# Kernel tuning notes

Measured on AMD Instinct MI355X. Metric: run time of the kernel, lower is better.

Reference implementation:

```python
import jax, jax.numpy as jnp
import numpy as np

B, T, D = 2, 2048, 2048
H, HKV, DH = 16, 4, 128  # n_heads, n_kv_heads, d_head
EPS = 1e-6


def _rms_norm(t):
    # normalize over last dim, no learned weight (matches F.rms_norm default)
    return t * jax.lax.rsqrt(jnp.mean(t * t, axis=-1, keepdims=True) + EPS)


def _ortho_rope(t, cos, sin):
    # t: (b, h, t, d); unfold(-1,2,2) -> even/odd pairs
    x0 = t[..., 0::2]  # (b,h,t,d/2)
    x1 = t[..., 1::2]
    y0 = x0 * cos - x1 * sin
    y1 = x1 * cos + x0 * sin
    # NOTE: concatenated halves (NOT re-interleaved), faithful to source
    return jnp.concatenate((y0, y1), axis=-1)


def setup_inputs() -> dict:
    key = jax.random.key(0)
    ks = jax.random.split(key, 10)
    return {
        "x": jax.random.normal(ks[0], (B, T, D), jnp.float32),
        "pos_ids": jnp.broadcast_to(jnp.arange(T, dtype=jnp.int64), (B, T)),
        "cos": jax.random.normal(ks[1], (T, DH // 2), jnp.float32),
        "sin": jax.random.normal(ks[2], (T, DH // 2), jnp.float32),
        "v1": jax.random.normal(ks[3], (B, HKV, T, DH), jnp.float32),
        "Wq": jax.random.normal(ks[4], (H * DH, D), jnp.float32) * (D ** -0.5),
        "Wk": jax.random.normal(ks[5], (HKV * DH, D), jnp.float32) * (D ** -0.5),
        "Wv": jax.random.normal(ks[6], (HKV * DH, D), jnp.float32) * (D ** -0.5),
        "Wo": jax.random.normal(ks[7], (D, D), jnp.float32) * (D ** -0.5),
        "gate_w": jax.random.normal(ks[8], (H, H), jnp.float32) * 0.1,
        "v_lamb": jnp.float32(0.5),
    }


def reference(x, pos_ids, cos, sin, v1, Wq, Wk, Wv, Wo, gate_w, v_lamb):
    b, t, _ = x.shape
    # fused QKV projections (Linear, no bias: x @ W.T), split to heads
    q = (x @ Wq.T).reshape(b, t, H, DH).transpose(0, 2, 1, 3)    # (b,H,t,d)
    k = (x @ Wk.T).reshape(b, t, HKV, DH).transpose(0, 2, 1, 3)  # (b,Hkv,t,d)
    v = (x @ Wv.T).reshape(b, t, HKV, DH).transpose(0, 2, 1, 3)
    # value residual: lerp(v, v1, lamb) = v + lamb*(v1 - v)
    v = v + v_lamb * (v1 - v)
    # QK RMSNorm then ortho RoPE
    q = _ortho_rope(_rms_norm(q), cos, sin)
    k = _ortho_rope(_rms_norm(k), cos, sin)
    # kv_cache.upsert modeled as prefill: k,v unchanged, causal block mask
    g = H // HKV  # GQA group size
    k = jnp.repeat(k, g, axis=1)  # (b,H,t,d)
    vfull = jnp.repeat(v, g, axis=1)
    scale = DH ** -0.5
    scores = jnp.einsum('bhqd,bhkd->bhqk', q, k) * scale
    causal = jnp.tril(jnp.ones((t, t), dtype=bool))
    scores = jnp.where(causal, scores, jnp.finfo(scores.dtype).min)
    attn = jax.nn.softmax(scores, axis=-1)
    y = jnp.einsum('bhqk,bhkd->bhqd', attn, vfull)  # (b,H,t,d)
    # per-head sigmoid gate from first n_heads channels of x
    gates = jax.nn.sigmoid(x[..., :H] @ gate_w.T)   # (b,t,H)
    y = y * gates.transpose(0, 2, 1)[..., None]     # (b,H,t,1)
    y = y.transpose(0, 2, 1, 3).reshape(b, t, H * DH)
    out = y @ Wo.T
    return (out, v1)
```

## Files before the change

### kernel.cpp

```cpp
#include <hip/hip_runtime.h>

typedef __bf16 bf16;
typedef __attribute__((ext_vector_type(8))) __bf16 bf16x8;
typedef __attribute__((ext_vector_type(4))) __bf16 bf16x4;
typedef __attribute__((ext_vector_type(4))) float f32x4;
typedef __attribute__((ext_vector_type(4))) short short4v;

#define BB 2
#define TT 2048
#define DD 2048
#define HH 16
#define HKV 4
#define DHD 128
#define NQKV 3072

__device__ __forceinline__ void gl_lds16(const bf16* g, bf16* l) {
    __builtin_amdgcn_global_load_lds(
        (const __attribute__((address_space(1))) void*)g,
        (__attribute__((address_space(3))) void*)l, 16, 0, 0);
}

__global__ void cvt_bf16(const float* __restrict__ src, bf16* __restrict__ dst, int n8) {
    int i = blockIdx.x * 256 + threadIdx.x;
    if (i >= n8) return;
    float4 a = ((const float4*)src)[i * 2];
    float4 b = ((const float4*)src)[i * 2 + 1];
    bf16x8 v;
    v[0] = (bf16)a.x; v[1] = (bf16)a.y; v[2] = (bf16)a.z; v[3] = (bf16)a.w;
    v[4] = (bf16)b.x; v[5] = (bf16)b.y; v[6] = (bf16)b.z; v[7] = (bf16)b.w;
    *(bf16x8*)(dst + (size_t)i * 8) = v;
}

template <int MODE>
__global__ void gemm_bt(const bf16* __restrict__ A, const bf16* __restrict__ Bw,
                        int M, int N, int K,
                        float* __restrict__ Cout,
                        bf16* __restrict__ qb, bf16* __restrict__ kb,
                        bf16* __restrict__ vtb,
                        const float* __restrict__ v1,
                        const float* __restrict__ cosb,
                        const float* __restrict__ sinb,
                        const float* __restrict__ lamp) {
    constexpr int SMEM_ELE = (MODE == 1) ? 17920 : 16384;
    __shared__ bf16 smem[SMEM_ELE];
    bf16* As = smem;
    bf16* Bs = smem + 8192;
    const int tid = threadIdx.x;
    const int w = tid >> 6, lane = tid & 63;
    const int l15 = lane & 15, quad = lane >> 4;

    const int nwg = gridDim.x * gridDim.y;
    int wg = blockIdx.y * gridDim.x + blockIdx.x;
    int swz = (wg & 7) * (nwg >> 3) + (wg >> 3);
    const int bx = swz % gridDim.x, by = swz / gridDim.x;
    const int m0 = by * 128, n0 = bx * 128;
    const int wm = (w & 1) * 64, wn = (w >> 1) * 64;

    f32x4 acc[4][4] = {};
    const int lrow = lane >> 2;
    const int scol = ((lane & 3) ^ ((lane >> 3) & 3)) * 8;
    const int xs = (quad ^ ((l15 >> 1) & 3)) * 8;

    for (int k0 = 0; k0 < K; k0 += 64) {
#pragma unroll
        for (int i = 0; i < 4; i++) {
            int c = w * 4 + i;
            int kc2 = c >> 3, rc = c & 7;
            int row = rc * 16 + lrow;
            int kk = k0 + kc2 * 32 + scol;
            gl_lds16(A + (size_t)(m0 + row) * K + kk, As + c * 512);
            gl_lds16(Bw + (size_t)(n0 + row) * K + kk, Bs + c * 512);
        }
        __syncthreads();
#pragma unroll
        for (int kc2 = 0; kc2 < 2; kc2++) {
            bf16x8 af[4], bfr[4];
#pragma unroll
            for (int mi = 0; mi < 4; mi++)
                af[mi] = *(const bf16x8*)(As + kc2 * 4096 + ((wm >> 4) + mi) * 512 + l15 * 32 + xs);
#pragma unroll
            for (int ni = 0; ni < 4; ni++)
                bfr[ni] = *(const bf16x8*)(Bs + kc2 * 4096 + ((wn >> 4) + ni) * 512 + l15 * 32 + xs);
#pragma unroll
            for (int mi = 0; mi < 4; mi++)
#pragma unroll
                for (int ni = 0; ni < 4; ni++)
                    acc[mi][ni] = __builtin_amdgcn_mfma_f32_16x16x32_bf16(af[mi], bfr[ni], acc[mi][ni], 0, 0, 0);
        }
        __syncthreads();
    }

    if constexpr (MODE == 0) {
#pragma unroll
        for (int mi = 0; mi < 4; mi++)
#pragma unroll
            for (int ni = 0; ni < 4; ni++)
#pragma unroll
                for (int r = 0; r < 4; r++) {
                    int m = m0 + wm + mi * 16 + quad * 4 + r;
                    int n = n0 + wn + ni * 16 + l15;
                    Cout[(size_t)m * N + n] = acc[mi][ni][r];
                }
    } else {
        const int hid = n0 >> 7;
        const int b = m0 >> 11;
        const int t0 = m0 & (TT - 1);
        bf16* ep = smem;

        if (hid < 20) {
            float* ssum = (float*)(smem + 17408);
            float ssq[4][4];
#pragma unroll
            for (int mi = 0; mi < 4; mi++)
#pragma unroll
                for (int r = 0; r < 4; r++) {
                    float s = 0.f;
#pragma unroll
                    for (int ni = 0; ni < 4; ni++) {
                        float v = acc[mi][ni][r];
                        s += v * v;
                    }
                    s += __shfl_xor(s, 1);
                    s += __shfl_xor(s, 2);
                    s += __shfl_xor(s, 4);
                    s += __shfl_xor(s, 8);
                    ssq[mi][r] = s;
                }
            if (l15 == 0) {
#pragma unroll
                for (int mi = 0; mi < 4; mi++)
#pragma unroll
                    for (int r = 0; r < 4; r++)
                        ssum[(wn >> 6) * 128 + wm + mi * 16 + quad * 4 + r] = ssq[mi][r];
            }
            __syncthreads();
            const float QSCALE = 0.08838834764831845f * 1.4426950408889634f;
            float rn[4][4];
#pragma unroll
            for (int mi = 0; mi < 4; mi++)
#pragma unroll
                for (int r = 0; r < 4; r++) {
                    int row = wm + mi * 16 + quad * 4 + r;
                    float ss = ssum[row] + ssum[128 + row];
                    float rv = rsqrtf(ss * (1.f / 128.f) + 1e-6f);
                    if (hid < HH) rv *= QSCALE;
                    rn[mi][r] = rv;
                }
#pragma unroll
            for (int mi = 0; mi < 4; mi++)
#pragma unroll
                for (int ni = 0; ni < 4; ni++)
#pragma unroll
                    for (int r = 0; r < 4; r++) {
                        float sv = acc[mi][ni][r] * rn[mi][r];
                        float pv = __shfl_xor(sv, 1);
                        int nl = wn + ni * 16 + l15;
                        int j = nl >> 1;
                        int tl = wm + mi * 16 + quad * 4 + r;
                        float c = cosb[(size_t)(t0 + tl) * 64 + j];
                        float s = sinb[(size_t)(t0 + tl) * 64 + j];
                        float o = (nl & 1) ? (sv * c + pv * s) : (sv * c - pv * s);
                        int oc = (nl & 1) ? (64 + j) : j;
                        ep[tl * 136 + oc] = (bf16)o;
                    }
            __syncthreads();
            bf16* dst = (hid < HH)
                ? (qb + ((size_t)(b * HH + hid) * TT + t0) * DHD)
                : (kb + ((size_t)(b * HKV + (hid - HH)) * TT + t0) * DHD);
            int tl = tid >> 1, half = tid & 1;
#pragma unroll
            for (int c8 = 0; c8 < 8; c8++)
                *(bf16x8*)(dst + (size_t)tl * DHD + half * 64 + c8 * 8) =
                    *(const bf16x8*)(ep + tl * 136 + half * 64 + c8 * 8);
        } else {
            float lam = lamp[0];
            int vh = hid - 20;
            const float* v1b = v1 + ((size_t)(b * HKV + vh) * TT) * DHD;
#pragma unroll
            for (int mi = 0; mi < 4; mi++)
#pragma unroll
                for (int ni = 0; ni < 4; ni++)
#pragma unroll
                    for (int r = 0; r < 4; r++) {
                        int d = wn + ni * 16 + l15;
                        int tl = wm + mi * 16 + quad * 4 + r;
                        float val = acc[mi][ni][r];
                        float vm = val + lam * (v1b[(size_t)(t0 + tl) * DHD + d] - val);
                        ep[d * 136 + tl] = (bf16)vm;
                    }
            __syncthreads();
            bf16* dstv = vtb + ((size_t)(b * HKV + vh) * DHD) * TT + t0;
            int dd = tid >> 1, half = tid & 1;
#pragma unroll
            for (int c8 = 0; c8 < 8; c8++)
                *(bf16x8*)(dstv + (size_t)dd * TT + half * 64 + c8 * 8) =
                    *(const bf16x8*)(ep + dd * 136 + half * 64 + c8 * 8);
        }
    }
}

__global__ void gatesk(const float* __restrict__ x, const float* __restrict__ gw,
                       float* __restrict__ gates) {
    __shared__ float gws[256];
    gws[threadIdx.x] = gw[threadIdx.x];
    __syncthreads();
    int idx = blockIdx.x * 256 + threadIdx.x;
    int h = idx & 15, token = idx >> 4;
    const float* xr = x + (size_t)token * DD;
    float z = 0.f;
#pragma unroll
    for (int j = 0; j < 16; j++) z += xr[j] * gws[h * 16 + j];
    gates[idx] = 1.f / (1.f + __expf(-z));
}

__global__ __launch_bounds__(512, 2) void fattn(const bf16* __restrict__ qbuf,
                                                const bf16* __restrict__ kbuf,
                                                const bf16* __restrict__ vt,
                                                const float* __restrict__ gates,
                                                bf16* __restrict__ yb) {
    __shared__ bf16 Ks[2][4 * 2048];
    __shared__ bf16 VTs[2][8192];

    const int bid = blockIdx.x;
    const int bh = bid & 31;
    const int g = bid >> 5;
    const int h = bh & 15, b = bh >> 4;
    const int hk = h >> 2;
    const int tid = threadIdx.x, w = tid >> 6, lane = tid & 63;
    const int wq = w & 3, grp = w >> 2;
    const int l15 = lane & 15, quad = lane >> 4;

    const bf16* qbase = qbuf + ((size_t)(b * HH + h) * TT) * DHD;
    const bf16* kbase = kbuf + ((size_t)(b * HKV + hk) * TT) * DHD;
    const bf16* vtbase = vt + ((size_t)(b * HKV + hk) * DHD) * TT;

    const int Tq0 = grp ? (15 - g) : g;
    const int Tq1 = grp ? (16 + g) : (31 - g);
    const int ktmax_blk = 31 - g;

    bf16x8 qf0[4], qf1[4];
#pragma unroll
    for (int kc = 0; kc < 4; kc++) {
        qf0[kc] = *(const bf16x8*)(qbase + (size_t)(Tq0 * 64 + wq * 16 + l15) * DHD + kc * 32 + quad * 8);
        qf1[kc] = *(const bf16x8*)(qbase + (size_t)(Tq1 * 64 + wq * 16 + l15) * DHD + kc * 32 + quad * 8);
    }

    bool dm[4][4];
#pragma unroll
    for (int ni = 0; ni < 4; ni++)
#pragma unroll
        for (int r = 0; r < 4; r++)
            dm[ni][r] = ((ni >> 1) * 32 + quad * 8 + (ni & 1) * 4 + r) > (wq * 16 + l15);

    const int srow = lane >> 2;
    const int gst = (((lane >> 5) & 1) << 1) | ((lane >> 3) & 1);
    const int scg = ((lane & 3) ^ gst) * 8;
    const int vrow = lane >> 3;
    const int vcg = ((lane & 7) ^ ((lane >> 3) & 7)) * 8;

    auto stage = [&](int kt, int buf) {
        if (grp == 0) {
#pragma unroll
            for (int i = 0; i < 4; i++)
                gl_lds16(kbase + (size_t)(kt * 64 + wq * 16 + srow) * DHD + i * 32 + scg,
                         &Ks[buf][i * 2048 + wq * 512]);
        } else {
#pragma unroll
            for (int i = 0; i < 4; i++)
                gl_lds16(vtbase + (size_t)(wq * 32 + i * 8 + vrow) * TT + kt * 64 + vcg,
                         &VTs[buf][wq * 2048 + i * 512]);
        }
    };

    stage(0, 0);

    const int gk = (((l15 >> 2) & 1) << 1) | ((l15 >> 1) & 1);

    f32x4 O0[8] = {}, O1[8] = {};
    float m0 = -INFINITY, l0 = 0.f, m1 = -INFINITY, l1 = 0.f;

    union PW { bf16x4 h[2]; bf16x8 v; };

    for (int kt = 0; kt <= ktmax_blk; kt++) {
        int cur = kt & 1;
        __syncthreads();
        if (kt < ktmax_blk) stage(kt + 1, cur ^ 1);

        if (kt > Tq1) continue;
        const bool a0 = (kt <= Tq0);

        f32x4 s0[4], s1[4];
        __builtin_amdgcn_s_setprio(1);
#pragma unroll
        for (int ni = 0; ni < 4; ni++) {
            int rr = (ni >> 1) * 32 + (l15 >> 2) * 8 + (ni & 1) * 4 + (l15 & 3);
            bf16x8 kfl[4];
#pragma unroll
            for (int kc = 0; kc < 4; kc++)
                kfl[kc] = *(const bf16x8*)(&Ks[cur][kc * 2048 + rr * 32 + ((quad ^ gk) * 8)]);
            f32x4 z1 = {};
#pragma unroll
            for (int kc = 0; kc < 4; kc++)
                z1 = __builtin_amdgcn_mfma_f32_16x16x32_bf16(kfl[kc], qf1[kc], z1, 0, 0, 0);
            s1[ni] = z1;
            if (a0) {
                f32x4 z0 = {};
#pragma unroll
                for (int kc = 0; kc < 4; kc++)
                    z0 = __builtin_amdgcn_mfma_f32_16x16x32_bf16(kfl[kc], qf0[kc], z0, 0, 0, 0);
                s0[ni] = z0;
            }
        }
        __builtin_amdgcn_s_setprio(0);

        PW pw0[2], pw1[2];
        {
            if (kt == Tq1) {
#pragma unroll
                for (int ni = 0; ni < 4; ni++)
#pragma unroll
                    for (int r = 0; r < 4; r++)
                        if (dm[ni][r]) s1[ni][r] = -INFINITY;
            }
            float mx = s1[0][0];
#pragma unroll
            for (int ni = 0; ni < 4; ni++)
#pragma unroll
                for (int r = 0; r < 4; r++) mx = fmaxf(mx, s1[ni][r]);
            mx = fmaxf(mx, __shfl_xor(mx, 16));
            mx = fmaxf(mx, __shfl_xor(mx, 32));
            float mold = m1;
            bool noresc = __all(mx <= mold + 8.f);
            float mnew = noresc ? mold : fmaxf(mold, mx);
            float rs = 0.f;
#pragma unroll
            for (int ni = 0; ni < 4; ni++) {
                bf16x4 hv;
#pragma unroll
                for (int r = 0; r < 4; r++) {
                    float pe = __builtin_amdgcn_exp2f(s1[ni][r] - mnew);
                    hv[r] = (bf16)pe;
                    rs += pe;
                }
                pw1[ni >> 1].h[ni & 1] = hv;
            }
            rs += __shfl_xor(rs, 16);
            rs += __shfl_xor(rs, 32);
            if (!noresc) {
                float al = __builtin_amdgcn_exp2f(mold - mnew);
                l1 *= al;
#pragma unroll
                for (int dn = 0; dn < 8; dn++)
#pragma unroll
                    for (int r = 0; r < 4; r++) O1[dn][r] *= al;
                m1 = mnew;
            }
            l1 += rs;
        }
        if (a0) {
            if (kt == Tq0) {
#pragma unroll
                for (int ni = 0; ni < 4; ni++)
#pragma unroll
                    for (int r = 0; r < 4; r++)
                        if (dm[ni][r]) s0[ni][r] = -INFINITY;
            }
            float mx = s0[0][0];
#pragma unroll
            for (int ni = 0; ni < 4; ni++)
#pragma unroll
                for (int r = 0; r < 4; r++) mx = fmaxf(mx, s0[ni][r]);
            mx = fmaxf(mx, __shfl_xor(mx, 16));
            mx = fmaxf(mx, __shfl_xor(mx, 32));
            float mold = m0;
            bool noresc = __all(mx <= mold + 8.f);
            float mnew = noresc ? mold : fmaxf(mold, mx);
            float rs = 0.f;
#pragma unroll
            for (int ni = 0; ni < 4; ni++) {
                bf16x4 hv;
#pragma unroll
                for (int r = 0; r < 4; r++) {
                    float pe = __builtin_amdgcn_exp2f(s0[ni][r] - mnew);
                    hv[r] = (bf16)pe;
                    rs += pe;
                }
                pw0[ni >> 1].h[ni & 1] = hv;
            }
            rs += __shfl_xor(rs, 16);
            rs += __shfl_xor(rs, 32);
            if (!noresc) {
                float al = __builtin_amdgcn_exp2f(mold - mnew);
                l0 *= al;
#pragma unroll
                for (int dn = 0; dn < 8; dn++)
#pragma unroll
                    for (int r = 0; r < 4; r++) O0[dn][r] *= al;
                m0 = mnew;
            }
            l0 += rs;
        }

        __builtin_amdgcn_s_setprio(1);
#pragma unroll
        for (int ni2 = 0; ni2 < 2; ni2++) {
            bf16x8 vfl[8];
#pragma unroll
            for (int dn = 0; dn < 8; dn++)
                vfl[dn] = *(const bf16x8*)(&VTs[cur][(dn * 16 + l15) * 64 +
                                                    (((ni2 * 4 + quad) ^ (l15 & 7)) * 8)]);
#pragma unroll
            for (int dn = 0; dn < 8; dn++)
                O1[dn] = __builtin_amdgcn_mfma_f32_16x16x32_bf16(vfl[dn], pw1[ni2].v, O1[dn], 0, 0, 0);
            if (a0) {
#pragma unroll
                for (int dn = 0; dn < 8; dn++)
                    O0[dn] = __builtin_amdgcn_mfma_f32_16x16x32_bf16(vfl[dn], pw0[ni2].v, O0[dn], 0, 0, 0);
            }
        }
        __builtin_amdgcn_s_setprio(0);
    }

    auto epi = [&](const f32x4* Oc, float lsum, int qt) {
        int qg = qt * 64 + wq * 16 + l15;
        float gi = gates[((size_t)b * TT + qg) * HH + h] / lsum;
#pragma unroll
        for (int dn = 0; dn < 8; dn++) {
            bf16x4 o;
#pragma unroll
            for (int r = 0; r < 4; r++) o[r] = (bf16)(Oc[dn][r] * gi);
            *(bf16x4*)(yb + ((size_t)(b * TT + qg) * HH + h) * DHD + dn * 16 + quad * 4) = o;
        }
    };
    epi(O0, l0, Tq0);
    epi(O1, l1, Tq1);
}

extern "C" void kernel_launch(void* const* d_in, const int* in_sizes, int n_in,
                              void* d_out, int out_size, void* d_ws, size_t ws_size,
                              hipStream_t stream) {
    const float* x    = (const float*)d_in[0];
    const float* cosb = (const float*)d_in[2];
    const float* sinb = (const float*)d_in[3];
    const float* v1   = (const float*)d_in[4];
    const float* Wq   = (const float*)d_in[5];
    const float* Wk   = (const float*)d_in[6];
    const float* Wv   = (const float*)d_in[7];
    const float* Wo   = (const float*)d_in[8];
    const float* gw   = (const float*)d_in[9];
    const float* lam  = (const float*)d_in[10];
    float* out = (float*)d_out;

    char* ws = (char*)d_ws;
    bf16* xb     = (bf16*)(ws);
    bf16* wqkvb  = (bf16*)(ws + 16777216);
    bf16* wob    = (bf16*)(ws + 29360128);
    bf16* qb     = (bf16*)(ws + 79691776);
    bf16* kb     = (bf16*)(ws + 96468992);
    bf16* vtb    = (bf16*)(ws + 100663296);
    float* gts   = (float*)(ws + 104857600);
    bf16* yb     = xb;

    cvt_bf16<<<4096, 256, 0, stream>>>(x, xb, 1048576);
    cvt_bf16<<<2048, 256, 0, stream>>>(Wq, wqkvb, 524288);
    cvt_bf16<<<512, 256, 0, stream>>>(Wk, wqkvb + 4194304, 131072);
    cvt_bf16<<<512, 256, 0, stream>>>(Wv, wqkvb + 5242880, 131072);
    cvt_bf16<<<2048, 256, 0, stream>>>(Wo, wob, 524288);

    gemm_bt<1><<<dim3(24, 32), 256, 0, stream>>>(xb, wqkvb, 4096, NQKV, 2048,
                                                 nullptr, qb, kb, vtb, v1,
                                                 cosb, sinb, lam);
    gatesk<<<256, 256, 0, stream>>>(x, gw, gts);
    fattn<<<256, 512, 0, stream>>>(qb, kb, vtb, gts, yb);
    gemm_bt<0><<<dim3(16, 32), 256, 0, stream>>>(yb, wob, 4096, 2048, 2048,
                                                 out, nullptr, nullptr, nullptr,
                                                 nullptr, nullptr, nullptr, nullptr);
    (void)hipMemcpyAsync(out + 8388608, v1, (size_t)2097152 * sizeof(float),
                         hipMemcpyDeviceToDevice, stream);
}
```

Before: 303.3 us.

## Fuse conversion launches with gate computation and fold v1 copy into attention

Merges the five fp32-to-bf16 conversion launches into one kernel that also computes the sigmoid head gates, since each x block of 2048 elements is exactly one token row. This drops the separate gates kernel. The v1 passthrough copy moves from a device-to-device memcpy into the start of the attention kernel, where each block copies an 8192-float slice. The intent is to cut launch overhead and the separate copy pass, at the cost of extra memory traffic at the start of attention.

Result: faster. 292.5 us (-3.6%).

```diff
diff --git a/kernel.cpp b/kernel.cpp
--- a/kernel.cpp
+++ b/kernel.cpp
@@ -20,15 +20,44 @@
         (__attribute__((address_space(3))) void*)l, 16, 0, 0);
 }
 
-__global__ void cvt_bf16(const float* __restrict__ src, bf16* __restrict__ dst, int n8) {
-    int i = blockIdx.x * 256 + threadIdx.x;
-    if (i >= n8) return;
+__global__ void cvt_fuse(const float* __restrict__ x, const float* __restrict__ Wq,
+                         const float* __restrict__ Wk, const float* __restrict__ Wv,
+                         const float* __restrict__ Wo, const float* __restrict__ gw,
+                         bf16* __restrict__ xb, bf16* __restrict__ wqkvb,
+                         bf16* __restrict__ wob, float* __restrict__ gates) {
+    const int blk = blockIdx.x, tid = threadIdx.x;
+    const float* src; bf16* dst; int i;
+    const bool isx = blk < 4096;
+    if (isx)              { src = x;  dst = xb;              i = blk * 256 + tid; }
+    else if (blk < 6144)  { src = Wq; dst = wqkvb;           i = (blk - 4096) * 256 + tid; }
+    else if (blk < 6656)  { src = Wk; dst = wqkvb + 4194304; i = (blk - 6144) * 256 + tid; }
+    else if (blk < 7168)  { src = Wv; dst = wqkvb + 5242880; i = (blk - 6656) * 256 + tid; }
+    else                  { src = Wo; dst = wob;             i = (blk - 7168) * 256 + tid; }
     float4 a = ((const float4*)src)[i * 2];
     float4 b = ((const float4*)src)[i * 2 + 1];
     bf16x8 v;
     v[0] = (bf16)a.x; v[1] = (bf16)a.y; v[2] = (bf16)a.z; v[3] = (bf16)a.w;
     v[4] = (bf16)b.x; v[5] = (bf16)b.y; v[6] = (bf16)b.z; v[7] = (bf16)b.w;
     *(bf16x8*)(dst + (size_t)i * 8) = v;
+
+    if (isx) {
+        __shared__ float xs16[16];
+        __shared__ float gws[256];
+        gws[tid] = gw[tid];
+        if (tid < 2) {
+            xs16[tid * 8 + 0] = a.x; xs16[tid * 8 + 1] = a.y;
+            xs16[tid * 8 + 2] = a.z; xs16[tid * 8 + 3] = a.w;
+            xs16[tid * 8 + 4] = b.x; xs16[tid * 8 + 5] = b.y;
+            xs16[tid * 8 + 6] = b.z; xs16[tid * 8 + 7] = b.w;
+        }
+        __syncthreads();
+        if (tid < 16) {
+            float z = 0.f;
+#pragma unroll
+            for (int j = 0; j < 16; j++) z += xs16[j] * gws[tid * 16 + j];
+            gates[blk * 16 + tid] = 1.f / (1.f + __expf(-z));
+        }
+    }
 }
 
 template <int MODE>
@@ -179,15 +208,15 @@
 #pragma unroll
             for (int mi = 0; mi < 4; mi++)
 #pragma unroll
-                for (int ni = 0; ni < 4; ni++)
-#pragma unroll
-                    for (int r = 0; r < 4; r++) {
-                        int d = wn + ni * 16 + l15;
-                        int tl = wm + mi * 16 + quad * 4 + r;
-                        float val = acc[mi][ni][r];
-                        float vm = val + lam * (v1b[(size_t)(t0 + tl) * DHD + d] - val);
-                        ep[d * 136 + tl] = (bf16)vm;
-                    }
+            for (int ni = 0; ni < 4; ni++)
+#pragma unroll
+                for (int r = 0; r < 4; r++) {
+                    int d = wn + ni * 16 + l15;
+                    int tl = wm + mi * 16 + quad * 4 + r;
+                    float val = acc[mi][ni][r];
+                    float vm = val + lam * (v1b[(size_t)(t0 + tl) * DHD + d] - val);
+                    ep[d * 136 + tl] = (bf16)vm;
+                }
             __syncthreads();
             bf16* dstv = vtb + ((size_t)(b * HKV + vh) * DHD) * TT + t0;
             int dd = tid >> 1, half = tid & 1;
@@ -197,27 +226,15 @@
                     *(const bf16x8*)(ep + dd * 136 + half * 64 + c8 * 8);
         }
     }
-}
-
-__global__ void gatesk(const float* __restrict__ x, const float* __restrict__ gw,
-                       float* __restrict__ gates) {
-    __shared__ float gws[256];
-    gws[threadIdx.x] = gw[threadIdx.x];
-    __syncthreads();
-    int idx = blockIdx.x * 256 + threadIdx.x;
-    int h = idx & 15, token = idx >> 4;
-    const float* xr = x + (size_t)token * DD;
-    float z = 0.f;
-#pragma unroll
-    for (int j = 0; j < 16; j++) z += xr[j] * gws[h * 16 + j];
-    gates[idx] = 1.f / (1.f + __expf(-z));
 }
 
 __global__ __launch_bounds__(512, 2) void fattn(const bf16* __restrict__ qbuf,
                                                 const bf16* __restrict__ kbuf,
                                                 const bf16* __restrict__ vt,
                                                 const float* __restrict__ gates,
-                                                bf16* __restrict__ yb) {
+                                                bf16* __restrict__ yb,
+                                                const float* __restrict__ v1f,
+                                                float* __restrict__ vout) {
     __shared__ bf16 Ks[2][4 * 2048];
     __shared__ bf16 VTs[2][8192];
 
@@ -229,6 +246,13 @@
     const int tid = threadIdx.x, w = tid >> 6, lane = tid & 63;
     const int wq = w & 3, grp = w >> 2;
     const int l15 = lane & 15, quad = lane >> 4;
+
+    {
+        const float4* s4 = (const float4*)(v1f + (size_t)bid * 8192);
+        float4* d4 = (float4*)(vout + (size_t)bid * 8192);
+#pragma unroll
+        for (int i = 0; i < 4; i++) d4[tid + i * 512] = s4[tid + i * 512];
+    }
 
     const bf16* qbase = qbuf + ((size_t)(b * HH + h) * TT) * DHD;
     const bf16* kbase = kbuf + ((size_t)(b * HKV + hk) * TT) * DHD;
@@ -461,20 +485,13 @@
     float* gts   = (float*)(ws + 104857600);
     bf16* yb     = xb;
 
-    cvt_bf16<<<4096, 256, 0, stream>>>(x, xb, 1048576);
-    cvt_bf16<<<2048, 256, 0, stream>>>(Wq, wqkvb, 524288);
-    cvt_bf16<<<512, 256, 0, stream>>>(Wk, wqkvb + 4194304, 131072);
-    cvt_bf16<<<512, 256, 0, stream>>>(Wv, wqkvb + 5242880, 131072);
-    cvt_bf16<<<2048, 256, 0, stream>>>(Wo, wob, 524288);
+    cvt_fuse<<<9216, 256, 0, stream>>>(x, Wq, Wk, Wv, Wo, gw, xb, wqkvb, wob, gts);
 
     gemm_bt<1><<<dim3(24, 32), 256, 0, stream>>>(xb, wqkvb, 4096, NQKV, 2048,
                                                  nullptr, qb, kb, vtb, v1,
                                                  cosb, sinb, lam);
-    gatesk<<<256, 256, 0, stream>>>(x, gw, gts);
-    fattn<<<256, 512, 0, stream>>>(qb, kb, vtb, gts, yb);
+    fattn<<<256, 512, 0, stream>>>(qb, kb, vtb, gts, yb, v1, out + 8388608);
     gemm_bt<0><<<dim3(16, 32), 256, 0, stream>>>(yb, wob, 4096, 2048, 2048,
                                                  out, nullptr, nullptr, nullptr,
                                                  nullptr, nullptr, nullptr, nullptr);
-    (void)hipMemcpyAsync(out + 8388608, v1, (size_t)2097152 * sizeof(float),
-                         hipMemcpyDeviceToDevice, stream);
 }
```
